# Kernel optimization log

Hardware: AMD Instinct MI355X
Metric: run time of the kernel (lower is better)

Reference implementation:

```python
import jax, jax.numpy as jnp
import numpy as np

N_NODES = 50000
N_EDGES = 1500000
FEAT = 128
CUTOFF = 5.0


def setup_inputs() -> dict:
    key = jax.random.key(0)
    k_x, k_ei, k_el, k_w = jax.random.split(key, 4)
    x = jax.random.normal(k_x, (N_NODES, FEAT), dtype=jnp.float32)
    edge_index = jax.random.randint(k_ei, (2, N_EDGES), 0, N_NODES, dtype=jnp.int64)
    edge_len = jax.random.uniform(k_el, (N_EDGES,), dtype=jnp.float32) * CUTOFF
    # learned params: equivariant mix (dense linear for scalar irreps, no bias),
    # log of distance scale (init sharpness=6.0), and 1->1 filter linear.
    W_mix = jax.random.normal(k_w, (FEAT, FEAT), dtype=jnp.float32) / np.sqrt(FEAT)
    log_scale = jnp.asarray(np.log(6.0), dtype=jnp.float32)
    filter_w = jnp.asarray(0.7, dtype=jnp.float32)
    filter_b = jnp.asarray(0.1, dtype=jnp.float32)
    return {"x": x, "edge_index": edge_index, "edge_len": edge_len,
            "W_mix": W_mix, "log_scale": log_scale,
            "filter_w": filter_w, "filter_b": filter_b}


def reference(x, edge_index, edge_len, W_mix, log_scale, filter_w, filter_b):
    sender = edge_index[0]
    receiver = edge_index[1]
    n_nodes = x.shape[0]

    scale = jnp.exp(log_scale).astype(edge_len.dtype)
    decay = jnp.exp(-jnp.maximum(edge_len / (scale + 1e-6), 0.0) ** 2)  # [E]
    gate = jax.nn.sigmoid(edge_len * filter_w + filter_b)               # [E]
    weights = jnp.nan_to_num(decay * gate, nan=0.0, posinf=0.0, neginf=0.0)

    # gather-scale-scatter: messages [E, F] -> per-node sum
    messages = weights[:, None].astype(x.dtype) * x[sender]
    agg = jax.ops.segment_sum(messages, receiver, num_segments=n_nodes)
    degree = jax.ops.segment_sum(jnp.ones_like(edge_len), receiver,
                                 num_segments=n_nodes)
    agg = agg / jnp.maximum(degree, 1.0)[:, None].astype(x.dtype)

    return x + agg @ W_mix
```

## Files before the change

kernel.cpp:

```cpp
#include <hip/hip_runtime.h>
#include <math.h>

#define FEAT 128
#define BSHIFT 5
#define BNODES 32
#define CAP 2048
#define NBUCK_MAX 2048

__device__ __forceinline__ float edge_weight(float d, float scale, float fw, float fb) {
    float t = fmaxf(d / scale, 0.0f);
    float decay = expf(-t * t);
    float g = 1.0f / (1.0f + expf(-(d * fw + fb)));
    float w = decay * g;
    if (!isfinite(w)) w = 0.0f;
    return w;
}

__device__ __forceinline__ unsigned int bf16_rne(float f) {
    unsigned int b = __float_as_uint(f);
    return (b + 0x7FFFu + ((b >> 16) & 1u)) >> 16;
}

__global__ __launch_bounds__(256) void convert_kernel(const float4* __restrict__ x4,
                                                      uint2* __restrict__ xbf,
                                                      int n4) {
    int i = blockIdx.x * 256 + threadIdx.x;
    if (i >= n4) return;
    float4 v = x4[i];
    uint2 o;
    o.x = (bf16_rne(v.y) << 16) | bf16_rne(v.x);
    o.y = (bf16_rne(v.w) << 16) | bf16_rne(v.z);
    xbf[i] = o;
}

__global__ __launch_bounds__(256) void count_kernel(const int* __restrict__ recv,
                                                    int* __restrict__ sub,
                                                    int E, int nbuck, int epb) {
    __shared__ int cnt[NBUCK_MAX];
    int tid = threadIdx.x;
    for (int i = tid; i < nbuck; i += 256) cnt[i] = 0;
    __syncthreads();
    int base = blockIdx.x * epb;
    int end = min(base + epb, E);
    for (int e = base + tid; e < end; e += 256)
        atomicAdd(&cnt[recv[e] >> BSHIFT], 1);
    __syncthreads();
    size_t row = (size_t)blockIdx.x * nbuck;
    for (int i = tid; i < nbuck; i += 256) sub[row + i] = cnt[i];
}

__global__ __launch_bounds__(256) void colscan_kernel(int* __restrict__ sub,
                                                      int* __restrict__ tot,
                                                      int nbuck, int nchunk) {
    __shared__ int vals[256];
    int b = blockIdx.x;
    int tid = threadIdx.x;
    int carry = 0;
    for (int c0 = 0; c0 < nchunk; c0 += 256) {
        int c = c0 + tid;
        int v = (c < nchunk) ? sub[(size_t)c * nbuck + b] : 0;
        vals[tid] = v;
        __syncthreads();
        for (int d = 1; d < 256; d <<= 1) {
            int t = (tid >= d) ? vals[tid - d] : 0;
            __syncthreads();
            vals[tid] += t;
            __syncthreads();
        }
        int excl = vals[tid] - v;
        if (c < nchunk) sub[(size_t)c * nbuck + b] = carry + excl;
        int btot = vals[255];
        __syncthreads();
        carry += btot;
    }
    if (tid == 0) tot[b] = carry;
}

__global__ __launch_bounds__(1024) void scan_kernel(const int* __restrict__ tot,
                                                    int* __restrict__ boff, int M) {
    __shared__ int part[1024];
    int t = threadIdx.x;
    int chunk = (M + 1023) >> 10;
    int lo = t * chunk, hi = min(lo + chunk, M);
    int s = 0;
    for (int i = lo; i < hi; ++i) s += tot[i];
    part[t] = s;
    __syncthreads();
    for (int d = 1; d < 1024; d <<= 1) {
        int v = (t >= d) ? part[t - d] : 0;
        __syncthreads();
        part[t] += v;
        __syncthreads();
    }
    int run = part[t] - s;
    for (int i = lo; i < hi; ++i) {
        boff[i] = run;
        run += tot[i];
    }
    if (hi == M) boff[M] = run;
}

__global__ __launch_bounds__(256) void bucket_scatter_kernel(
    const int* __restrict__ sender, const int* __restrict__ recv,
    const float* __restrict__ edge_len,
    const float* __restrict__ log_scale, const float* __restrict__ filter_w,
    const float* __restrict__ filter_b,
    const int* __restrict__ sub, const int* __restrict__ boff,
    unsigned long long* __restrict__ buf, int E, int nbuck, int epb) {
    __shared__ int cur[NBUCK_MAX];
    int tid = threadIdx.x;
    size_t row = (size_t)blockIdx.x * nbuck;
    for (int i = tid; i < nbuck; i += 256) cur[i] = boff[i] + sub[row + i];
    __syncthreads();
    int base = blockIdx.x * epb;
    int end = min(base + epb, E);
    float scale = expf(log_scale[0]) + 1e-6f;
    float fw = filter_w[0], fb = filter_b[0];
    for (int e = base + tid; e < end; e += 256) {
        int r = recv[e];
        int s = sender[e];
        float w = edge_weight(edge_len[e], scale, fw, fb);
        int pos = atomicAdd(&cur[r >> BSHIFT], 1);
        unsigned long long rec = ((unsigned long long)__float_as_uint(w) << 32)
                               | (unsigned int)(s & 0xFFFF)
                               | ((unsigned int)(r & (BNODES - 1)) << 16);
        buf[pos] = rec;
    }
}

__device__ __forceinline__ void accum8(float acc[8], uint4 u, float w) {
    acc[0] = fmaf(w, __uint_as_float(u.x << 16), acc[0]);
    acc[1] = fmaf(w, __uint_as_float(u.x & 0xFFFF0000u), acc[1]);
    acc[2] = fmaf(w, __uint_as_float(u.y << 16), acc[2]);
    acc[3] = fmaf(w, __uint_as_float(u.y & 0xFFFF0000u), acc[3]);
    acc[4] = fmaf(w, __uint_as_float(u.z << 16), acc[4]);
    acc[5] = fmaf(w, __uint_as_float(u.z & 0xFFFF0000u), acc[5]);
    acc[6] = fmaf(w, __uint_as_float(u.w << 16), acc[6]);
    acc[7] = fmaf(w, __uint_as_float(u.w & 0xFFFF0000u), acc[7]);
}

__global__ __launch_bounds__(256) void bucket_sort_aggregate_kernel(
    const uint4* __restrict__ xbf4, const unsigned long long* __restrict__ buf,
    const int* __restrict__ boff, uint4* __restrict__ agg_bf4,
    int* __restrict__ deg, int N) {
    __shared__ unsigned long long recS[CAP];
    __shared__ int cnt32[BNODES];
    __shared__ int segoff[BNODES + 1];

    int b = blockIdx.x;
    int n0 = b << BSHIFT;
    int nEnd = min(n0 + BNODES, N);
    int lo = boff[b], hi = boff[b + 1];
    int tid = threadIdx.x;
    int lane = tid & 15;
    int grp = tid >> 4;

    float acc[2][8] = {{0.f,0.f,0.f,0.f,0.f,0.f,0.f,0.f},
                       {0.f,0.f,0.f,0.f,0.f,0.f,0.f,0.f}};
    int dcnt[2] = {0, 0};

    for (int pos = lo; pos < hi; pos += CAP) {
        int cnt = min(CAP, hi - pos);
        if (tid < BNODES) cnt32[tid] = 0;
        __syncthreads();

        unsigned long long rec[CAP / 256];
        int rnk[CAP / 256];
        int locl[CAP / 256];
#pragma unroll
        for (int k = 0; k < CAP / 256; ++k) {
            int i = k * 256 + tid;
            if (i < cnt) {
                unsigned long long r = buf[pos + i];
                int l = ((unsigned int)r >> 16) & (BNODES - 1);
                rec[k] = r;
                locl[k] = l;
                rnk[k] = atomicAdd(&cnt32[l], 1);
            }
        }
        __syncthreads();
        if (tid == 0) {
            int run = 0;
#pragma unroll
            for (int l = 0; l < BNODES; ++l) { segoff[l] = run; run += cnt32[l]; }
            segoff[BNODES] = run;
        }
        __syncthreads();
#pragma unroll
        for (int k = 0; k < CAP / 256; ++k) {
            int i = k * 256 + tid;
            if (i < cnt) recS[segoff[locl[k]] + rnk[k]] = rec[k];
        }
        __syncthreads();

#pragma unroll
        for (int which = 0; which < 2; ++which) {
            int l = grp + which * 16;
            int s0 = segoff[l], s1 = segoff[l + 1];
            dcnt[which] += s1 - s0;
            int i = s0;
            for (; i + 4 <= s1; i += 4) {
                unsigned long long r0 = recS[i];
                unsigned long long r1 = recS[i + 1];
                unsigned long long r2 = recS[i + 2];
                unsigned long long r3 = recS[i + 3];
                float w0 = __uint_as_float((unsigned int)(r0 >> 32));
                float w1 = __uint_as_float((unsigned int)(r1 >> 32));
                float w2 = __uint_as_float((unsigned int)(r2 >> 32));
                float w3 = __uint_as_float((unsigned int)(r3 >> 32));
                int s0i = (unsigned int)r0 & 0xFFFF;
                int s1i = (unsigned int)r1 & 0xFFFF;
                int s2i = (unsigned int)r2 & 0xFFFF;
                int s3i = (unsigned int)r3 & 0xFFFF;
                uint4 u0 = xbf4[(size_t)s0i * 16 + lane];
                uint4 u1 = xbf4[(size_t)s1i * 16 + lane];
                uint4 u2 = xbf4[(size_t)s2i * 16 + lane];
                uint4 u3 = xbf4[(size_t)s3i * 16 + lane];
                accum8(acc[which], u0, w0);
                accum8(acc[which], u1, w1);
                accum8(acc[which], u2, w2);
                accum8(acc[which], u3, w3);
            }
            for (; i < s1; ++i) {
                unsigned long long ra = recS[i];
                float wa = __uint_as_float((unsigned int)(ra >> 32));
                int sa = (unsigned int)ra & 0xFFFF;
                uint4 ua = xbf4[(size_t)sa * 16 + lane];
                accum8(acc[which], ua, wa);
            }
        }
        __syncthreads();
    }

#pragma unroll
    for (int which = 0; which < 2; ++which) {
        int n = n0 + grp + which * 16;
        if (n < nEnd) {
            uint4 o;
            o.x = (bf16_rne(acc[which][1]) << 16) | bf16_rne(acc[which][0]);
            o.y = (bf16_rne(acc[which][3]) << 16) | bf16_rne(acc[which][2]);
            o.z = (bf16_rne(acc[which][5]) << 16) | bf16_rne(acc[which][4]);
            o.w = (bf16_rne(acc[which][7]) << 16) | bf16_rne(acc[which][6]);
            agg_bf4[(size_t)n * 16 + lane] = o;
            if (lane == 0) deg[n] = dcnt[which];
        }
    }
}

__global__ __launch_bounds__(256) void finalize_kernel(
    const float* __restrict__ x, const uint4* __restrict__ agg_bf4,
    const int* __restrict__ deg, const float* __restrict__ Wm,
    float* __restrict__ out, int N) {
    __shared__ float aggS[64 * 128];
    __shared__ float Ws[128 * 64];
    const int n0 = blockIdx.x * 64;

    for (int i = threadIdx.x; i < 64 * 16; i += 256) {
        int r = i >> 4;
        int q = i & 15;
        int n = n0 + r;
        uint4 u = make_uint4(0u, 0u, 0u, 0u);
        if (n < N) u = agg_bf4[(size_t)n * 16 + q];
        float4 f0, f1;
        f0.x = __uint_as_float(u.x << 16);
        f0.y = __uint_as_float(u.x & 0xFFFF0000u);
        f0.z = __uint_as_float(u.y << 16);
        f0.w = __uint_as_float(u.y & 0xFFFF0000u);
        f1.x = __uint_as_float(u.z << 16);
        f1.y = __uint_as_float(u.z & 0xFFFF0000u);
        f1.z = __uint_as_float(u.w << 16);
        f1.w = __uint_as_float(u.w & 0xFFFF0000u);
        int m = (r >> 2) & 7;
        ((float4*)aggS)[r * 32 + ((2 * q) ^ m)] = f0;
        ((float4*)aggS)[r * 32 + ((2 * q + 1) ^ m)] = f1;
    }

    const int tc = threadIdx.x & 15;
    const int tr = threadIdx.x >> 4;

    float invd[4];
#pragma unroll
    for (int i = 0; i < 4; ++i) {
        int n = n0 + 4 * tr + i;
        float degf = 1.0f;
        if (n < N) degf = fmaxf((float)deg[n], 1.0f);
        invd[i] = 1.0f / degf;
    }

    for (int h = 0; h < 2; ++h) {
        for (int i = threadIdx.x; i < 128 * 16; i += 256) {
            int k = i >> 4;
            int j4 = i & 15;
            ((float4*)Ws)[k * 16 + j4] = ((const float4*)Wm)[k * 32 + h * 16 + j4];
        }
        __syncthreads();

        float acc[4][4];
#pragma unroll
        for (int i = 0; i < 4; ++i)
#pragma unroll
            for (int c = 0; c < 4; ++c) acc[i][c] = 0.f;

#pragma unroll 4
        for (int k0 = 0; k0 < 128; k0 += 4) {
            float4 ar4[4];
            const int chunk = (k0 >> 2) ^ (tr & 7);
#pragma unroll
            for (int i = 0; i < 4; ++i) {
                int r = 4 * tr + i;
                ar4[i] = ((const float4*)aggS)[r * 32 + chunk];
            }
            float4 wv4[4];
#pragma unroll
            for (int kk = 0; kk < 4; ++kk)
                wv4[kk] = *(const float4*)&Ws[(k0 + kk) * 64 + tc * 4];

            float wvv[4][4];
#pragma unroll
            for (int kk = 0; kk < 4; ++kk) {
                wvv[kk][0] = wv4[kk].x; wvv[kk][1] = wv4[kk].y;
                wvv[kk][2] = wv4[kk].z; wvv[kk][3] = wv4[kk].w;
            }
#pragma unroll
            for (int i = 0; i < 4; ++i) {
                float av[4] = {ar4[i].x, ar4[i].y, ar4[i].z, ar4[i].w};
#pragma unroll
                for (int kk = 0; kk < 4; ++kk)
#pragma unroll
                    for (int c = 0; c < 4; ++c)
                        acc[i][c] = fmaf(av[kk], wvv[kk][c], acc[i][c]);
            }
        }

#pragma unroll
        for (int i = 0; i < 4; ++i) {
            int n = n0 + 4 * tr + i;
            if (n < N) {
                size_t base = (size_t)n * FEAT + h * 64 + tc * 4;
                float4 xv = *(const float4*)&x[base];
                float4 o;
                o.x = xv.x + invd[i] * acc[i][0];
                o.y = xv.y + invd[i] * acc[i][1];
                o.z = xv.z + invd[i] * acc[i][2];
                o.w = xv.w + invd[i] * acc[i][3];
                *(float4*)&out[base] = o;
            }
        }
        __syncthreads();
    }
}

__global__ __launch_bounds__(256) void scatter_fallback(
    const float4* __restrict__ x4, const int* __restrict__ sender,
    const int* __restrict__ receiver, const float* __restrict__ edge_len,
    const float* __restrict__ log_scale, const float* __restrict__ filter_w,
    const float* __restrict__ filter_b, float* __restrict__ agg,
    float* __restrict__ deg, int E) {
    int gid = blockIdx.x * 256 + threadIdx.x;
    int e = gid >> 5;
    if (e >= E) return;
    int lane = gid & 31;
    int s = sender[e];
    int r = receiver[e];
    float scale = expf(log_scale[0]) + 1e-6f;
    float w = edge_weight(edge_len[e], scale, filter_w[0], filter_b[0]);
    float4 xv = x4[s * (FEAT / 4) + lane];
    float* dst = agg + (size_t)r * FEAT + lane * 4;
    unsafeAtomicAdd(dst + 0, w * xv.x);
    unsafeAtomicAdd(dst + 1, w * xv.y);
    unsafeAtomicAdd(dst + 2, w * xv.z);
    unsafeAtomicAdd(dst + 3, w * xv.w);
    if (lane == 0) unsafeAtomicAdd(&deg[r], 1.0f);
}

__global__ __launch_bounds__(256) void finalize_fallback(
    const float* __restrict__ x, const float* __restrict__ agg,
    const float* __restrict__ deg, const float* __restrict__ Wm,
    float* __restrict__ out, int N) {
    __shared__ float Wsf[FEAT * FEAT];
    for (int i = threadIdx.x * 4; i < FEAT * FEAT; i += 256 * 4)
        *(float4*)&Wsf[i] = *(const float4*)&Wm[i];
    __syncthreads();
    int half = threadIdx.x >> 7;
    int j = threadIdx.x & (FEAT - 1);
    for (int n0 = blockIdx.x * 2; n0 < N; n0 += gridDim.x * 2) {
        int n = n0 + half;
        if (n < N) {
            const float* arow = agg + (size_t)n * FEAT;
            float acc = 0.0f;
#pragma unroll 16
            for (int k = 0; k < FEAT; ++k) acc = fmaf(arow[k], Wsf[k * FEAT + j], acc);
            float invd = 1.0f / fmaxf(deg[n], 1.0f);
            size_t idx = (size_t)n * FEAT + j;
            out[idx] = x[idx] + invd * acc;
        }
    }
}

extern "C" void kernel_launch(void* const* d_in, const int* in_sizes, int n_in,
                              void* d_out, int out_size, void* d_ws, size_t ws_size,
                              hipStream_t stream) {
    const float* x         = (const float*)d_in[0];
    const int*   ei        = (const int*)d_in[1];
    const float* edge_len  = (const float*)d_in[2];
    const float* W_mix     = (const float*)d_in[3];
    const float* log_scale = (const float*)d_in[4];
    const float* filter_w  = (const float*)d_in[5];
    const float* filter_b  = (const float*)d_in[6];
    float* out = (float*)d_out;

    const int N = in_sizes[0] / FEAT;
    const int E = in_sizes[1] / 2;
    const int* sender   = ei;
    const int* receiver = ei + E;
    const int nbuck = (N + BNODES - 1) >> BSHIFT;

    size_t xbf_bytes  = (size_t)N * FEAT * 2;
    size_t aggb_bytes = (size_t)N * FEAT * 2;
    size_t buf_bytes  = (size_t)E * 8;
    size_t tot_bytes  = (((size_t)nbuck * 4) + 63) & ~(size_t)63;
    size_t boff_bytes = (((size_t)(nbuck + 1) * 4) + 63) & ~(size_t)63;
    size_t deg_bytes  = (((size_t)N * 4) + 63) & ~(size_t)63;
    size_t fixed = xbf_bytes + aggb_bytes + buf_bytes + tot_bytes + boff_bytes +
                   deg_bytes;

    int epb = 0, nchunk = 0;
    size_t sub_bytes = 0;
    const int epb_opts[3] = {4096, 8192, 16384};
    for (int oi = 0; oi < 3; ++oi) {
        int cand = epb_opts[oi];
        int nc = (E + cand - 1) / cand;
        size_t sb = (((size_t)nc * nbuck * 4) + 63) & ~(size_t)63;
        if (fixed + sb <= ws_size) { epb = cand; nchunk = nc; sub_bytes = sb; break; }
    }

    if (epb != 0 && N <= 65536) {
        char* p = (char*)d_ws;
        uint2* xbf    = (uint2*)p;                        p += xbf_bytes;
        uint4* agg_bf = (uint4*)p;                        p += aggb_bytes;
        unsigned long long* buf = (unsigned long long*)p; p += buf_bytes;
        int* sub  = (int*)p;                              p += sub_bytes;
        int* tot  = (int*)p;                              p += tot_bytes;
        int* boff = (int*)p;                              p += boff_bytes;
        int* deg  = (int*)p;

        int cblocks = (N * (FEAT / 4) + 255) / 256;
        convert_kernel<<<cblocks, 256, 0, stream>>>((const float4*)x, xbf,
                                                    N * (FEAT / 4));
        count_kernel<<<nchunk, 256, 0, stream>>>(receiver, sub, E, nbuck, epb);
        colscan_kernel<<<nbuck, 256, 0, stream>>>(sub, tot, nbuck, nchunk);
        scan_kernel<<<1, 1024, 0, stream>>>(tot, boff, nbuck);
        bucket_scatter_kernel<<<nchunk, 256, 0, stream>>>(
            sender, receiver, edge_len, log_scale, filter_w, filter_b,
            sub, boff, buf, E, nbuck, epb);
        bucket_sort_aggregate_kernel<<<nbuck, 256, 0, stream>>>(
            (const uint4*)xbf, buf, boff, agg_bf, deg, N);
        int fblocks = (N + 63) / 64;
        finalize_kernel<<<fblocks, 256, 0, stream>>>(x, (const uint4*)agg_bf, deg,
                                                     W_mix, out, N);
    } else {
        float* agg = (float*)d_ws;
        float* degf = agg + (size_t)N * FEAT;
        hipMemsetAsync(agg, 0, ((size_t)N * FEAT + N) * sizeof(float), stream);
        int sblocks = (E * 32 + 255) / 256;
        scatter_fallback<<<sblocks, 256, 0, stream>>>(
            (const float4*)x, sender, receiver, edge_len,
            log_scale, filter_w, filter_b, agg, degf, E);
        finalize_fallback<<<512, 256, 0, stream>>>(x, agg, degf, W_mix, out, N);
    }
}
```

Measured before the change: 231.8 us.

## Shrink node buckets to 16 and merge convert and count kernels

Bucket size drops from 32 to 16 nodes, with CAP halved and the bucket limit doubled. The aggregate kernel now has one node per 16-lane group and twice as many blocks, which should improve parallelism and occupancy. The bf16 convert and receiver-count kernels are merged into a single launch that branches on blockIdx, removing one launch and letting the two run concurrently. In exchange, the count and scan stages work with twice as many buckets, a larger shared count array, and more sub-matrix traffic.

```diff
diff --git a/kernel.cpp b/kernel.cpp
--- a/kernel.cpp
+++ b/kernel.cpp
@@ -2,10 +2,10 @@
 #include <math.h>
 
 #define FEAT 128
-#define BSHIFT 5
-#define BNODES 32
-#define CAP 2048
-#define NBUCK_MAX 2048
+#define BSHIFT 4
+#define BNODES 16
+#define CAP 1024
+#define NBUCK_MAX 4096
 
 __device__ __forceinline__ float edge_weight(float d, float scale, float fw, float fb) {
     float t = fmaxf(d / scale, 0.0f);
@@ -21,32 +21,32 @@
     return (b + 0x7FFFu + ((b >> 16) & 1u)) >> 16;
 }
 
-__global__ __launch_bounds__(256) void convert_kernel(const float4* __restrict__ x4,
-                                                      uint2* __restrict__ xbf,
-                                                      int n4) {
-    int i = blockIdx.x * 256 + threadIdx.x;
-    if (i >= n4) return;
-    float4 v = x4[i];
-    uint2 o;
-    o.x = (bf16_rne(v.y) << 16) | bf16_rne(v.x);
-    o.y = (bf16_rne(v.w) << 16) | bf16_rne(v.z);
-    xbf[i] = o;
-}
-
-__global__ __launch_bounds__(256) void count_kernel(const int* __restrict__ recv,
-                                                    int* __restrict__ sub,
-                                                    int E, int nbuck, int epb) {
+__global__ __launch_bounds__(256) void convert_count_kernel(
+    const float4* __restrict__ x4, uint2* __restrict__ xbf, int n4,
+    const int* __restrict__ recv, int* __restrict__ sub,
+    int E, int nbuck, int epb, int cblocks) {
     __shared__ int cnt[NBUCK_MAX];
-    int tid = threadIdx.x;
-    for (int i = tid; i < nbuck; i += 256) cnt[i] = 0;
-    __syncthreads();
-    int base = blockIdx.x * epb;
-    int end = min(base + epb, E);
-    for (int e = base + tid; e < end; e += 256)
-        atomicAdd(&cnt[recv[e] >> BSHIFT], 1);
-    __syncthreads();
-    size_t row = (size_t)blockIdx.x * nbuck;
-    for (int i = tid; i < nbuck; i += 256) sub[row + i] = cnt[i];
+    if ((int)blockIdx.x < cblocks) {
+        int i = blockIdx.x * 256 + threadIdx.x;
+        if (i >= n4) return;
+        float4 v = x4[i];
+        uint2 o;
+        o.x = (bf16_rne(v.y) << 16) | bf16_rne(v.x);
+        o.y = (bf16_rne(v.w) << 16) | bf16_rne(v.z);
+        xbf[i] = o;
+    } else {
+        int cb = blockIdx.x - cblocks;
+        int tid = threadIdx.x;
+        for (int i = tid; i < nbuck; i += 256) cnt[i] = 0;
+        __syncthreads();
+        int base = cb * epb;
+        int end = min(base + epb, E);
+        for (int e = base + tid; e < end; e += 256)
+            atomicAdd(&cnt[recv[e] >> BSHIFT], 1);
+        __syncthreads();
+        size_t row = (size_t)cb * nbuck;
+        for (int i = tid; i < nbuck; i += 256) sub[row + i] = cnt[i];
+    }
 }
 
 __global__ __launch_bounds__(256) void colscan_kernel(int* __restrict__ sub,
@@ -144,7 +144,7 @@
     const int* __restrict__ boff, uint4* __restrict__ agg_bf4,
     int* __restrict__ deg, int N) {
     __shared__ unsigned long long recS[CAP];
-    __shared__ int cnt32[BNODES];
+    __shared__ int cnt16[BNODES];
     __shared__ int segoff[BNODES + 1];
 
     int b = blockIdx.x;
@@ -155,13 +155,12 @@
     int lane = tid & 15;
     int grp = tid >> 4;
 
-    float acc[2][8] = {{0.f,0.f,0.f,0.f,0.f,0.f,0.f,0.f},
-                       {0.f,0.f,0.f,0.f,0.f,0.f,0.f,0.f}};
-    int dcnt[2] = {0, 0};
+    float acc[8] = {0.f, 0.f, 0.f, 0.f, 0.f, 0.f, 0.f, 0.f};
+    int dcnt = 0;
 
     for (int pos = lo; pos < hi; pos += CAP) {
         int cnt = min(CAP, hi - pos);
-        if (tid < BNODES) cnt32[tid] = 0;
+        if (tid < BNODES) cnt16[tid] = 0;
         __syncthreads();
 
         unsigned long long rec[CAP / 256];
@@ -175,14 +174,14 @@
                 int l = ((unsigned int)r >> 16) & (BNODES - 1);
                 rec[k] = r;
                 locl[k] = l;
-                rnk[k] = atomicAdd(&cnt32[l], 1);
+                rnk[k] = atomicAdd(&cnt16[l], 1);
             }
         }
         __syncthreads();
         if (tid == 0) {
             int run = 0;
 #pragma unroll
-            for (int l = 0; l < BNODES; ++l) { segoff[l] = run; run += cnt32[l]; }
+            for (int l = 0; l < BNODES; ++l) { segoff[l] = run; run += cnt16[l]; }
             segoff[BNODES] = run;
         }
         __syncthreads();
@@ -193,11 +192,9 @@
         }
         __syncthreads();
 
-#pragma unroll
-        for (int which = 0; which < 2; ++which) {
-            int l = grp + which * 16;
-            int s0 = segoff[l], s1 = segoff[l + 1];
-            dcnt[which] += s1 - s0;
+        {
+            int s0 = segoff[grp], s1 = segoff[grp + 1];
+            dcnt += s1 - s0;
             int i = s0;
             for (; i + 4 <= s1; i += 4) {
                 unsigned long long r0 = recS[i];
@@ -216,34 +213,31 @@
                 uint4 u1 = xbf4[(size_t)s1i * 16 + lane];
                 uint4 u2 = xbf4[(size_t)s2i * 16 + lane];
                 uint4 u3 = xbf4[(size_t)s3i * 16 + lane];
-                accum8(acc[which], u0, w0);
-                accum8(acc[which], u1, w1);
-                accum8(acc[which], u2, w2);
-                accum8(acc[which], u3, w3);
+                accum8(acc, u0, w0);
+                accum8(acc, u1, w1);
+                accum8(acc, u2, w2);
+                accum8(acc, u3, w3);
             }
             for (; i < s1; ++i) {
                 unsigned long long ra = recS[i];
                 float wa = __uint_as_float((unsigned int)(ra >> 32));
                 int sa = (unsigned int)ra & 0xFFFF;
                 uint4 ua = xbf4[(size_t)sa * 16 + lane];
-                accum8(acc[which], ua, wa);
-            }
-        }
-        __syncthreads();
-    }
-
-#pragma unroll
-    for (int which = 0; which < 2; ++which) {
-        int n = n0 + grp + which * 16;
-        if (n < nEnd) {
-            uint4 o;
-            o.x = (bf16_rne(acc[which][1]) << 16) | bf16_rne(acc[which][0]);
-            o.y = (bf16_rne(acc[which][3]) << 16) | bf16_rne(acc[which][2]);
-            o.z = (bf16_rne(acc[which][5]) << 16) | bf16_rne(acc[which][4]);
-            o.w = (bf16_rne(acc[which][7]) << 16) | bf16_rne(acc[which][6]);
-            agg_bf4[(size_t)n * 16 + lane] = o;
-            if (lane == 0) deg[n] = dcnt[which];
-        }
+                accum8(acc, ua, wa);
+            }
+        }
+        __syncthreads();
+    }
+
+    int n = n0 + grp;
+    if (n < nEnd) {
+        uint4 o;
+        o.x = (bf16_rne(acc[1]) << 16) | bf16_rne(acc[0]);
+        o.y = (bf16_rne(acc[3]) << 16) | bf16_rne(acc[2]);
+        o.z = (bf16_rne(acc[5]) << 16) | bf16_rne(acc[4]);
+        o.w = (bf16_rne(acc[7]) << 16) | bf16_rne(acc[6]);
+        agg_bf4[(size_t)n * 16 + lane] = o;
+        if (lane == 0) deg[n] = dcnt;
     }
 }
 
@@ -445,9 +439,9 @@
         int* deg  = (int*)p;
 
         int cblocks = (N * (FEAT / 4) + 255) / 256;
-        convert_kernel<<<cblocks, 256, 0, stream>>>((const float4*)x, xbf,
-                                                    N * (FEAT / 4));
-        count_kernel<<<nchunk, 256, 0, stream>>>(receiver, sub, E, nbuck, epb);
+        convert_count_kernel<<<cblocks + nchunk, 256, 0, stream>>>(
+            (const float4*)x, xbf, N * (FEAT / 4),
+            receiver, sub, E, nbuck, epb, cblocks);
         colscan_kernel<<<nbuck, 256, 0, stream>>>(sub, tot, nbuck, nchunk);
         scan_kernel<<<1, 1024, 0, stream>>>(tot, boff, nbuck);
         bucket_scatter_kernel<<<nchunk, 256, 0, stream>>>(
```

New measurement: 241.4 us. 1.04x slower.
